# Optimization experiments

Measured on AMD Instinct MI355X. Metric: run time of the kernel, lower is better.

The kernel has to match this reference:

```python
import jax, jax.numpy as jnp
import numpy as np
from jax import lax

B, N, NPOINT = 16, 4096, 512
C_FEAT = 64
RADII = (0.2, 0.4)
NSAMPLES = (32, 64)
LAYER_DIMS = ([64, 64, 128], [64, 96, 128])  # hidden dims + feat_size per scale
C_IN = C_FEAT + 3  # use_xyz_feature=True prepends relative xyz
EPS = 1e-5


def setup_inputs() -> dict:
    key = jax.random.key(0)
    ks = jax.random.split(key, 32)
    inp = {
        "xyz": jax.random.uniform(ks[0], (B, N, 3), jnp.float32),
        "features": jax.random.normal(ks[1], (B, C_FEAT, N), jnp.float32),
    }
    ki = 2
    for s, dims in enumerate(LAYER_DIMS):
        full = [C_IN] + list(dims)
        for l in range(len(full) - 1):
            cin, cout = full[l], full[l + 1]
            inp["w_%d_%d" % (s, l)] = jax.random.normal(ks[ki], (cout, cin), jnp.float32) * np.float32(1.0 / np.sqrt(cin))
            inp["b_%d_%d" % (s, l)] = jnp.zeros((cout,), jnp.float32)
            inp["g_%d_%d" % (s, l)] = jnp.ones((cout,), jnp.float32)
            inp["beta_%d_%d" % (s, l)] = jnp.zeros((cout,), jnp.float32)
            ki += 1
    return inp


def _fps(xyz, npoint):
    # iterative farthest point sampling -> (B, npoint) int32 indices
    b, n, _ = xyz.shape
    init_idx = jnp.zeros((b,), jnp.int32)
    d0 = jnp.full((b, n), 1e10, xyz.dtype)

    def body(carry, _):
        dists, last = carry
        p = jnp.take_along_axis(xyz, last[:, None, None], axis=1)  # (B,1,3)
        dists = jnp.minimum(dists, jnp.sum((xyz - p) ** 2, -1))
        nxt = jnp.argmax(dists, -1).astype(jnp.int32)
        return (dists, nxt), nxt

    _, rest = lax.scan(body, (d0, init_idx), None, length=npoint - 1)
    return jnp.concatenate([init_idx[None, :], rest], 0).T


def _ball_query(xyz, new_xyz, radius, nsample):
    # first-nsample-in-order ball query, padded with first hit (CUDA ball_query semantics)
    n = xyz.shape[1]
    d2 = jnp.sum((new_xyz[:, :, None, :] - xyz[:, None, :, :]) ** 2, -1)  # (B,S,N)
    cand = jnp.where(d2 < radius * radius, jnp.arange(n, dtype=jnp.int32)[None, None, :], n)
    idx = jnp.sort(cand, axis=-1)[..., :nsample]
    first = idx[..., :1]
    idx = jnp.where(idx == n, first, idx)
    return jnp.minimum(idx, n - 1)


def _gather_pts(pts, idx):
    # pts (B,N,D), idx (B,...) -> (B,...,D)
    return jax.vmap(lambda p, i: p[i])(pts, idx)


def _scale(xyz, new_xyz, features, radius, nsample, params):
    idx = _ball_query(xyz, new_xyz, radius, nsample)  # (B,S,K)
    g_xyz = _gather_pts(xyz, idx) - new_xyz[:, :, None, :]  # (B,S,K,3) relative coords
    g_feat = jax.vmap(lambda f, i: f[:, i])(features, idx)  # (B,C,S,K)
    x = jnp.concatenate([g_xyz, jnp.transpose(g_feat, (0, 2, 3, 1))], -1)  # (B,S,K,3+C)
    nl = len(params)
    for li, (w, bb, gg, bt) in enumerate(params):
        # Conv1d(k=1) == per-point linear; BatchNorm1d train-mode stats over (batch*group, sample)
        x = jnp.einsum('bskc,oc->bsko', x, w) + bb
        mu = x.mean((0, 1, 2))
        var = x.var((0, 1, 2))
        x = (x - mu) * (gg / jnp.sqrt(var + EPS)) + bt
        if li < nl - 1:
            x = jax.nn.relu(x)
    # per-group max pool over samples -> (B,Cout,S)
    return jnp.transpose(x.max(2), (0, 2, 1))


def _forward(xyz, features, params_all):
    fps_idx = _fps(xyz, NPOINT)
    new_xyz = _gather_pts(xyz, fps_idx)  # (B,NPOINT,3)
    outs = [_scale(xyz, new_xyz, features, RADII[s], NSAMPLES[s], params_all[s]) for s in range(len(RADII))]
    return new_xyz, jnp.concatenate(outs, 1)  # (B,NPOINT,3), (B,256,NPOINT)


def reference(xyz, features,
              w_0_0, b_0_0, g_0_0, beta_0_0,
              w_0_1, b_0_1, g_0_1, beta_0_1,
              w_0_2, b_0_2, g_0_2, beta_0_2,
              w_1_0, b_1_0, g_1_0, beta_1_0,
              w_1_1, b_1_1, g_1_1, beta_1_1,
              w_1_2, b_1_2, g_1_2, beta_1_2):
    p0 = [(w_0_0, b_0_0, g_0_0, beta_0_0), (w_0_1, b_0_1, g_0_1, beta_0_1), (w_0_2, b_0_2, g_0_2, beta_0_2)]
    p1 = [(w_1_0, b_1_0, g_1_0, beta_1_0), (w_1_1, b_1_1, g_1_1, beta_1_1), (w_1_2, b_1_2, g_1_2, beta_1_2)]
    return _forward(xyz, features, [p0, p1])
```

## Files before the change

### kernel.cpp

```cpp
#include <hip/hip_runtime.h>

#define DEV __device__ __forceinline__

namespace {

typedef __attribute__((ext_vector_type(8))) short short8;
typedef __attribute__((ext_vector_type(4))) float f32x4;
typedef __attribute__((ext_vector_type(2))) float f32x2;

constexpr int B_ = 16, N_ = 4096, S_ = 512, CF_ = 64;
constexpr float EPS_ = 1e-5f;

constexpr int IDX0_OFF  = 0;
constexpr int IDX1_OFF  = 262144;
constexpr int STATS_OFF = IDX1_OFF + 524288;
constexpr int AC_OFF    = STATS_OFF + 49152;
constexpr int WP_OFF    = AC_OFF + 1536;
constexpr int MAXT_OFF  = WP_OFF + 21504;
constexpr int FEATT_OFF = MAXT_OFF + 1048576;
constexpr int Y0_OFF    = FEATT_OFF + 2097152;
constexpr int Y1_OFF    = Y0_OFF + 16777216;
constexpr size_t WS_NEED_FT   = (size_t)Y0_OFF * 4;
constexpr size_t WS_NEED_PIPE = (size_t)(Y1_OFF + 25165824) * 4;

constexpr int WP00 = 0,     WP01 = 6144,  WP02 = 10240;
constexpr int WP10 = 18432, WP11 = 24576, WP12 = 30720;

DEV int rfl(int x) { return __builtin_amdgcn_readfirstlane(x); }

DEV unsigned short f2bf(float x) {
  unsigned u = __float_as_uint(x);
  u += 0x7fff + ((u >> 16) & 1);
  return (unsigned short)(u >> 16);
}
DEV float bf2f(unsigned short u) { return __uint_as_float((unsigned)u << 16); }

DEV float dpp_max64(float v) {
  int m;
  m = __builtin_amdgcn_update_dpp(__float_as_int(v), __float_as_int(v), 0xB1, 0xf, 0xf, false);
  v = fmaxf(v, __int_as_float(m));
  m = __builtin_amdgcn_update_dpp(__float_as_int(v), __float_as_int(v), 0x4E, 0xf, 0xf, false);
  v = fmaxf(v, __int_as_float(m));
  m = __builtin_amdgcn_update_dpp(__float_as_int(v), __float_as_int(v), 0x141, 0xf, 0xf, false);
  v = fmaxf(v, __int_as_float(m));
  m = __builtin_amdgcn_update_dpp(__float_as_int(v), __float_as_int(v), 0x140, 0xf, 0xf, false);
  v = fmaxf(v, __int_as_float(m));
  m = __builtin_amdgcn_update_dpp(__float_as_int(v), __float_as_int(v), 0x142, 0xa, 0xf, false);
  v = fmaxf(v, __int_as_float(m));
  m = __builtin_amdgcn_update_dpp(__float_as_int(v), __float_as_int(v), 0x143, 0xc, 0xf, false);
  v = fmaxf(v, __int_as_float(m));
  return v;
}

__global__ __launch_bounds__(256) void fps_kernel(const float* __restrict__ xyz,
                                                  float* __restrict__ newxyz) {
  __shared__ float px[N_], py[N_], pz[N_];
  __shared__ unsigned long long swk[2][4];
  __shared__ int seq[S_];
  const int b = blockIdx.x, t = threadIdx.x;
  const int lane = t & 63, wv = t >> 6;
  const float* xb = xyz + (size_t)b * N_ * 3;
  for (int i = t; i < N_; i += 256) {
    px[i] = xb[i * 3 + 0];
    py[i] = xb[i * 3 + 1];
    pz[i] = xb[i * 3 + 2];
  }
  __syncthreads();
  f32x2 Xp[8], Yp[8], Zp[8], Dp[8];
#pragma unroll
  for (int jp = 0; jp < 8; ++jp) {
    Xp[jp] = *reinterpret_cast<const f32x2*>(&px[t * 16 + jp * 2]);
    Yp[jp] = *reinterpret_cast<const f32x2*>(&py[t * 16 + jp * 2]);
    Zp[jp] = *reinterpret_cast<const f32x2*>(&pz[t * 16 + jp * 2]);
    Dp[jp] = f32x2{1e10f, 1e10f};
  }
  float cx = px[0], cy = py[0], cz = pz[0];
  if (t == 0) seq[0] = 0;
  for (int it = 1; it < S_; ++it) {
    const int p = it & 1;
    f32x2 bvp = {-1.0f, -1.0f};
    {
#pragma clang fp contract(off)
      const f32x2 c2x = {cx, cx}, c2y = {cy, cy}, c2z = {cz, cz};
#pragma unroll
      for (int jp = 0; jp < 8; ++jp) {
        const f32x2 dx = Xp[jp] - c2x, dy = Yp[jp] - c2y, dz = Zp[jp] - c2z;
        const f32x2 d = (dx * dx + dy * dy) + dz * dz;
        Dp[jp] = __builtin_elementwise_min(Dp[jp], d);
        bvp = __builtin_elementwise_max(bvp, Dp[jp]);
      }
    }
    const float bv = fmaxf(bvp.x, bvp.y);
    int bj = 0;
#pragma unroll
    for (int j = 15; j >= 0; --j) {
      const float dj = Dp[j >> 1][j & 1];
      bj = (dj == bv) ? j : bj;
    }
    const int bi = t * 16 + bj;
    const float mxl = dpp_max64(bv);
    const float mx = __int_as_float(__builtin_amdgcn_readlane(__float_as_int(mxl), 63));
    const unsigned long long tie = __ballot(bv == mx);
    const int srcLane = (int)__builtin_ctzll(tie);
    const int wbi = __builtin_amdgcn_readlane(bi, srcLane);
    if (lane == 0)
      swk[p][wv] = ((unsigned long long)__float_as_uint(mx) << 32) | (unsigned)(~wbi);
    __syncthreads();
    const unsigned long long k0 = swk[p][0], k1 = swk[p][1];
    const unsigned long long k2 = swk[p][2], k3 = swk[p][3];
    const unsigned long long ka = k0 > k1 ? k0 : k1;
    const unsigned long long kb = k2 > k3 ? k2 : k3;
    const unsigned long long kw = ka > kb ? ka : kb;
    const int ri = (int)(~(unsigned)kw);
    cx = px[ri]; cy = py[ri]; cz = pz[ri];
    if (t == 0) seq[it] = ri;
  }
  __syncthreads();
  for (int i = t; i < S_; i += 256) {
    const int ri = seq[i];
    newxyz[(size_t)(b * S_ + i) * 3 + 0] = px[ri];
    newxyz[(size_t)(b * S_ + i) * 3 + 1] = py[ri];
    newxyz[(size_t)(b * S_ + i) * 3 + 2] = pz[ri];
  }
}

__global__ __launch_bounds__(256) void ballq_both(const float* __restrict__ xyz,
                                                  const float* __restrict__ newxyz,
                                                  int* __restrict__ idx0,
                                                  int* __restrict__ idx1) {
  __shared__ int sbuf[4][64];
  const int blk = blockIdx.x;
  const int scale = blk >> 11;
  const int cb = blk & 2047;
  const int NS = scale ? 64 : 32;
  const float r2 = scale ? 0.4f * 0.4f : 0.2f * 0.2f;
  int* __restrict__ idx = scale ? idx1 : idx0;
  const int wiv = threadIdx.x >> 6;
  const int lane = threadIdx.x & 63;
  const int cs = cb * 4 + wiv;
  const int b = cs >> 9;
  const float cx = newxyz[(size_t)cs * 3 + 0];
  const float cy = newxyz[(size_t)cs * 3 + 1];
  const float cz = newxyz[(size_t)cs * 3 + 2];
  const float* xb = xyz + (size_t)b * N_ * 3;
  int* my = sbuf[wiv];
  int cnt = 0;
  for (int base = 0; base < N_; base += 64) {
    if (cnt >= NS) break;
    const int i = base + lane;
    float d;
    {
#pragma clang fp contract(off)
      float dx = xb[i * 3 + 0] - cx, dy = xb[i * 3 + 1] - cy, dz = xb[i * 3 + 2] - cz;
      d = (dx * dx + dy * dy) + dz * dz;
    }
    const bool q = d < r2;
    const unsigned long long m = __ballot(q);
    if (q) {
      int pos = cnt + __popcll(m & ((1ull << lane) - 1ull));
      if (pos < NS) my[pos] = i;
    }
    cnt += __popcll(m);
  }
  __syncthreads();
  const int c = cnt < NS ? cnt : NS;
  const int first = my[0];
  for (int j = lane; j < NS; j += 64) idx[(size_t)cs * NS + j] = (j < c) ? my[j] : first;
}

__global__ __launch_bounds__(256) void prep_kernel(
    const float* __restrict__ feat, unsigned short* __restrict__ featT, int doFT,
    const float* __restrict__ w00, const float* __restrict__ w01, const float* __restrict__ w02,
    const float* __restrict__ w10, const float* __restrict__ w11, const float* __restrict__ w12,
    unsigned short* __restrict__ wp, float* __restrict__ stats) {
  const int blk = blockIdx.x, t = threadIdx.x;
  if (blk < 24) {
    for (int i = blk * 2048 + t; i < (blk + 1) * 2048; i += 256) stats[i] = 0.f;
  }
  {
    const int id = blk * 256 + t;
    const float* w = nullptr; int off = 0, KK = 0, CINW = 0, base = 0; bool perm = false;
    if (id < 768)       { w = w00; off = WP00; KK = 3; CINW = 67; perm = true;  base = 0; }
    else if (id < 1280) { w = w01; off = WP01; KK = 2; CINW = 64; perm = false; base = 768; }
    else if (id < 2304) { w = w02; off = WP02; KK = 2; CINW = 64; perm = false; base = 1280; }
    else if (id < 3072) { w = w10; off = WP10; KK = 3; CINW = 67; perm = true;  base = 2304; }
    else if (id < 3840) { w = w11; off = WP11; KK = 2; CINW = 64; perm = false; base = 3072; }
    else if (id < 5376) { w = w12; off = WP12; KK = 3; CINW = 96; perm = false; base = 3840; }
    if (w) {
      const int lid = id - base;
      const int lane = lid & 63, fr = lid >> 6;
      const int kk = fr % KK, nt = fr / KK;
      const int ccol = nt * 16 + (lane & 15);
      const int kbase = kk * 32 + (lane >> 4) * 8;
      unsigned short* dst = wp + off + (size_t)lid * 8;
#pragma unroll
      for (int j = 0; j < 8; ++j) {
        const int k = kbase + j;
        int cin;
        if (perm) cin = (k < 64) ? k + 3 : (k < 67 ? k - 64 : -1);
        else      cin = (k < CINW) ? k : -1;
        float f = (cin >= 0) ? w[ccol * CINW + cin] : 0.f;
        dst[j] = f2bf(f);
      }
    }
  }
  if (doFT) {
    __shared__ unsigned short tile[64][65];
    const int b = blk >> 6, nc = blk & 63;
    const int n0 = nc * 64;
    for (int i = t; i < 64 * 64; i += 256) {
      int c = i >> 6, n = i & 63;
      tile[c][n] = f2bf(feat[((size_t)b * CF_ + c) * N_ + n0 + n]);
    }
    __syncthreads();
    for (int i = t; i < 64 * 64; i += 256) {
      int n = i >> 6, c = i & 63;
      featT[((size_t)b * N_ + n0 + n) * 64 + c] = tile[c][n];
    }
  }
}

template <int DS>
DEV void flush_stats(const float* ssum, const float* ssq, int lane, int slot,
                     float* __restrict__ sg) {
  constexpr int NTS = DS / 16;
  float* dst = sg + (size_t)slot * 256;
#pragma unroll
  for (int nt = 0; nt < NTS; ++nt) {
    float s = ssum[nt], q = ssq[nt];
    s += __shfl_xor(s, 16); q += __shfl_xor(q, 16);
    s += __shfl_xor(s, 32); q += __shfl_xor(q, 32);
    if (lane < 16) {
      atomicAdd(&dst[nt * 16 + lane], s);
      atomicAdd(&dst[DS + nt * 16 + lane], q);
    }
  }
}

DEV void reduce_stats_block(const float* __restrict__ sg, float* sstats, int t) {
  float s = 0.f;
#pragma unroll
  for (int c = 0; c < 32; ++c) s += sg[c * 256 + t];
  sstats[t] = s;
  __syncthreads();
}

template <int K>
__global__ __launch_bounds__(256) void p1_kernel(
    const float* __restrict__ xyz, const unsigned short* __restrict__ featT,
    const float* __restrict__ newxyz, const int* __restrict__ idx,
    const unsigned short* __restrict__ wp0, const float* __restrict__ b0,
    unsigned short* __restrict__ y0, float* __restrict__ stats_out) {
  const int t = threadIdx.x, lane = t & 63;
  const int col = lane & 15, khi = lane >> 4;
  const int wid = rfl(t >> 6);
  constexpr int MT = (B_ * S_ * K) / 16;
  const int w0 = blockIdx.x * 4 + wid;
  short8 bfr[12];
#pragma unroll
  for (int i = 0; i < 12; ++i)
    bfr[i] = *reinterpret_cast<const short8*>(wp0 + ((size_t)i * 64 + lane) * 8);
  float bb[4];
#pragma unroll
  for (int nt = 0; nt < 4; ++nt) bb[nt] = b0[nt * 16 + col];
  float ssum[4] = {0.f, 0.f, 0.f, 0.f}, ssq[4] = {0.f, 0.f, 0.f, 0.f};
  for (int mt = w0; mt < MT; mt += 8192) {
    const int row = mt * 16 + col;
    const int cs = row / K;
    const int b = cs >> 9;
    const int pi = idx[row];
    const unsigned short* fr = featT + (((size_t)b * N_ + pi) << 6);
    const short8 a0 = *reinterpret_cast<const short8*>(fr + khi * 8);
    const short8 a1 = *reinterpret_cast<const short8*>(fr + 32 + khi * 8);
    short8 a2 = {0, 0, 0, 0, 0, 0, 0, 0};
    if (khi == 0) {
      const float* P = xyz + ((size_t)b * N_ + pi) * 3;
      const float* C = newxyz + (size_t)cs * 3;
      a2[0] = (short)f2bf(P[0] - C[0]);
      a2[1] = (short)f2bf(P[1] - C[1]);
      a2[2] = (short)f2bf(P[2] - C[2]);
    }
#pragma unroll
    for (int nt = 0; nt < 4; ++nt) {
      f32x4 a = {0.f, 0.f, 0.f, 0.f};
      a = __builtin_amdgcn_mfma_f32_16x16x32_bf16(a0, bfr[nt * 3 + 0], a, 0, 0, 0);
      a = __builtin_amdgcn_mfma_f32_16x16x32_bf16(a1, bfr[nt * 3 + 1], a, 0, 0, 0);
      a = __builtin_amdgcn_mfma_f32_16x16x32_bf16(a2, bfr[nt * 3 + 2], a, 0, 0, 0);
#pragma unroll
      for (int j = 0; j < 4; ++j) {
        const float y = a[j] + bb[nt];
        ssum[nt] += y; ssq[nt] += y * y;
        y0[(size_t)(mt * 16 + khi * 4 + j) * 64 + nt * 16 + col] = f2bf(y);
      }
    }
  }
  flush_stats<64>(ssum, ssq, lane, w0 & 31, stats_out);
}

template <int DIN, int DOUT>
__global__ __launch_bounds__(256) void p2_kernel(
    const unsigned short* __restrict__ yin, const unsigned short* __restrict__ wp,
    const float* __restrict__ bias, const float* __restrict__ gprev,
    const float* __restrict__ bprev, const float* __restrict__ stats_prev, float n,
    unsigned short* __restrict__ yout, float* __restrict__ stats_out, int MT) {
  constexpr int KK = DIN / 32, NT = DOUT / 16;
  __shared__ float sstats[256];
  const int t = threadIdx.x, lane = t & 63;
  const int col = lane & 15, khi = lane >> 4;
  const int wid = rfl(t >> 6);
  const int w0 = blockIdx.x * 4 + wid;
  reduce_stats_block(stats_prev, sstats, t);
  short8 bfr[NT * KK];
#pragma unroll
  for (int i = 0; i < NT * KK; ++i)
    bfr[i] = *reinterpret_cast<const short8*>(wp + ((size_t)i * 64 + lane) * 8);
  float bb[NT];
#pragma unroll
  for (int nt = 0; nt < NT; ++nt) bb[nt] = bias[nt * 16 + col];
  float ar[KK][8], cr[KK][8];
#pragma unroll
  for (int kk = 0; kk < KK; ++kk)
#pragma unroll
    for (int j = 0; j < 8; ++j) {
      const int ch = kk * 32 + khi * 8 + j;
      const float mu = sstats[ch] / n;
      const float var = sstats[DIN + ch] / n - mu * mu;
      const float a = gprev[ch] / sqrtf(var + EPS_);
      ar[kk][j] = a;
      cr[kk][j] = bprev[ch] - mu * a;
    }
  float ssum[NT], ssq[NT];
#pragma unroll
  for (int nt = 0; nt < NT; ++nt) { ssum[nt] = 0.f; ssq[nt] = 0.f; }
  for (int mt = w0; mt < MT; mt += 8192) {
    const size_t rb = (size_t)(mt * 16 + col) * DIN;
    short8 af[KK];
#pragma unroll
    for (int kk = 0; kk < KK; ++kk) {
      const short8 raw = *reinterpret_cast<const short8*>(yin + rb + kk * 32 + khi * 8);
#pragma unroll
      for (int j = 0; j < 8; ++j) {
        const float v = bf2f((unsigned short)raw[j]) * ar[kk][j] + cr[kk][j];
        af[kk][j] = (short)f2bf(fmaxf(v, 0.f));
      }
    }
#pragma unroll
    for (int nt = 0; nt < NT; ++nt) {
      f32x4 a = {0.f, 0.f, 0.f, 0.f};
#pragma unroll
      for (int kk = 0; kk < KK; ++kk)
        a = __builtin_amdgcn_mfma_f32_16x16x32_bf16(af[kk], bfr[nt * KK + kk], a, 0, 0, 0);
#pragma unroll
      for (int j = 0; j < 4; ++j) {
        const float y = a[j] + bb[nt];
        ssum[nt] += y; ssq[nt] += y * y;
        yout[(size_t)(mt * 16 + khi * 4 + j) * DOUT + nt * 16 + col] = f2bf(y);
      }
    }
  }
  flush_stats<DOUT>(ssum, ssq, lane, w0 & 31, stats_out);
}

template <int DIN, int K>
__global__ __launch_bounds__(256) void p3_kernel(
    const unsigned short* __restrict__ yin, const unsigned short* __restrict__ wp,
    const float* __restrict__ bias, const float* __restrict__ gprev,
    const float* __restrict__ bprev, const float* __restrict__ stats_prev, float n,
    float* __restrict__ maxtmp, float* __restrict__ stats_out) {
  constexpr int KK = DIN / 32, NT = 8;
  __shared__ float sstats[256];
  const int t = threadIdx.x, lane = t & 63;
  const int col = lane & 15, khi = lane >> 4;
  const int wid = rfl(t >> 6);
  const int c = blockIdx.x * 4 + wid;
  reduce_stats_block(stats_prev, sstats, t);
  short8 bfr[NT * KK];
#pragma unroll
  for (int i = 0; i < NT * KK; ++i)
    bfr[i] = *reinterpret_cast<const short8*>(wp + ((size_t)i * 64 + lane) * 8);
  float bb[NT];
#pragma unroll
  for (int nt = 0; nt < NT; ++nt) bb[nt] = bias[nt * 16 + col];
  float ar[KK][8], cr[KK][8];
#pragma unroll
  for (int kk = 0; kk < KK; ++kk)
#pragma unroll
    for (int j = 0; j < 8; ++j) {
      const int ch = kk * 32 + khi * 8 + j;
      const float mu = sstats[ch] / n;
      const float var = sstats[DIN + ch] / n - mu * mu;
      const float a = gprev[ch] / sqrtf(var + EPS_);
      ar[kk][j] = a;
      cr[kk][j] = bprev[ch] - mu * a;
    }
  float ssum[NT], ssq[NT], mx[NT];
#pragma unroll
  for (int nt = 0; nt < NT; ++nt) { ssum[nt] = 0.f; ssq[nt] = 0.f; mx[nt] = -3.4e38f; }
#pragma unroll
  for (int m = 0; m < K / 16; ++m) {
    const size_t rb = (size_t)(c * K + m * 16 + col) * DIN;
    short8 af[KK];
#pragma unroll
    for (int kk = 0; kk < KK; ++kk) {
      const short8 raw = *reinterpret_cast<const short8*>(yin + rb + kk * 32 + khi * 8);
#pragma unroll
      for (int j = 0; j < 8; ++j) {
        const float v = bf2f((unsigned short)raw[j]) * ar[kk][j] + cr[kk][j];
        af[kk][j] = (short)f2bf(fmaxf(v, 0.f));
      }
    }
#pragma unroll
    for (int nt = 0; nt < NT; ++nt) {
      f32x4 a = {0.f, 0.f, 0.f, 0.f};
#pragma unroll
      for (int kk = 0; kk < KK; ++kk)
        a = __builtin_amdgcn_mfma_f32_16x16x32_bf16(af[kk], bfr[nt * KK + kk], a, 0, 0, 0);
#pragma unroll
      for (int j = 0; j < 4; ++j) {
        const float y = a[j] + bb[nt];
        ssum[nt] += y; ssq[nt] += y * y;
        mx[nt] = fmaxf(mx[nt], y);
      }
    }
  }
#pragma unroll
  for (int nt = 0; nt < NT; ++nt) {
    mx[nt] = fmaxf(mx[nt], __shfl_xor(mx[nt], 16));
    mx[nt] = fmaxf(mx[nt], __shfl_xor(mx[nt], 32));
  }
  if (lane < 16) {
#pragma unroll
    for (int nt = 0; nt < NT; ++nt) maxtmp[(size_t)c * 128 + nt * 16 + lane] = mx[nt];
  }
  flush_stats<128>(ssum, ssq, lane, c & 31, stats_out);
}

__global__ __launch_bounds__(256) void out_kernel(const float* __restrict__ maxtmp,
                                                  const float* __restrict__ stats2,
                                                  const float* __restrict__ g2,
                                                  const float* __restrict__ be2, float n,
                                                  float* __restrict__ outf, int coff) {
  __shared__ float sstats[256];
  const int t = threadIdx.x;
  reduce_stats_block(stats2, sstats, t);
  const int i = blockIdx.x * 256 + t;
  if (i >= B_ * 128 * S_) return;
  const int s = i & 511;
  const int o = (i >> 9) & 127;
  const int b = i >> 16;
  const float mu = sstats[o] / n;
  const float var = sstats[128 + o] / n - mu * mu;
  const float a = g2[o] / sqrtf(var + EPS_);
  const float c = be2[o] - mu * a;
  const float v = maxtmp[((size_t)(b * S_ + s)) * 128 + o];
  outf[((size_t)b * 256 + coff + o) * S_ + s] = a * v + c;
}

template <int K, bool FT>
DEV void gather_tile(unsigned short* sX, const float* __restrict__ xyz,
                     const float* __restrict__ feat, const unsigned short* __restrict__ featT,
                     const float* __restrict__ newxyz, const int* __restrict__ idx, int tile) {
  const int t = threadIdx.x, r = t & 63, c4 = t >> 6;
  const int rep = r / K, k = r % K;
  const int cs = tile * (64 / K) + rep, b = cs >> 9;
  const int pi = idx[(size_t)cs * K + k];
  unsigned short* dst = sX + r * 104;
  if (FT) {
    const unsigned short* src = featT + (((size_t)b * N_ + pi) << 6) + c4 * 16;
    *reinterpret_cast<short8*>(dst + c4 * 16)     = *reinterpret_cast<const short8*>(src);
    *reinterpret_cast<short8*>(dst + c4 * 16 + 8) = *reinterpret_cast<const short8*>(src + 8);
  } else {
#pragma unroll
    for (int j = 0; j < 16; ++j) {
      const int ch = c4 * 16 + j;
      dst[ch] = f2bf(feat[((size_t)b * CF_ + ch) * N_ + pi]);
    }
  }
  if (c4 == 0) {
    const float* P = xyz + ((size_t)b * N_ + pi) * 3;
    const float* C = newxyz + (size_t)cs * 3;
    dst[64] = f2bf(P[0] - C[0]);
    dst[65] = f2bf(P[1] - C[1]);
    dst[66] = f2bf(P[2] - C[2]);
  }
}

template <int NTILES, int KK>
DEV void layer_mfma(const unsigned short* sIn, int stride, const unsigned short* __restrict__ wp,
                    int lane, int wid, f32x4* acc) {
  short8 af[KK];
  const int arow = wid * 16 + (lane & 15);
  const int kof = (lane >> 4) * 8;
#pragma unroll
  for (int kk = 0; kk < KK; ++kk)
    af[kk] = *reinterpret_cast<const short8*>(sIn + arow * stride + kk * 32 + kof);
#pragma unroll
  for (int nt = 0; nt < NTILES; ++nt) {
    f32x4 a = {0.f, 0.f, 0.f, 0.f};
#pragma unroll
    for (int kk = 0; kk < KK; ++kk) {
      short8 bf = *reinterpret_cast<const short8*>(wp + ((size_t)(nt * KK + kk) * 64 + lane) * 8);
      a = __builtin_amdgcn_mfma_f32_16x16x32_bf16(af[kk], bf, a, 0, 0, 0);
    }
    acc[nt] = a;
  }
}

template <int K, int D0, int D1, int D2, int STAGE, bool FT>
__global__ __launch_bounds__(256) void stage_mfma(
    const float* __restrict__ xyz, const float* __restrict__ feat,
    const unsigned short* __restrict__ featT, const float* __restrict__ newxyz,
    const int* __restrict__ idx,
    const unsigned short* __restrict__ wp0, const unsigned short* __restrict__ wp1,
    const unsigned short* __restrict__ wp2,
    const float* __restrict__ b0, const float* __restrict__ b1, const float* __restrict__ b2,
    const float* __restrict__ ac0, const float* __restrict__ ac1,
    float* __restrict__ stats_out, float* __restrict__ maxtmp) {
  constexpr int CPB = 64 / K, NT = (B_ * S_) / CPB;
  constexpr int ST0 = 104, ST1 = 72, ST2 = (D1 == 96) ? 104 : 72;
  constexpr int KK0 = 3, KK1 = D0 / 32, KK2 = D1 / 32;
  constexpr int NT0 = D0 / 16, NT1 = D1 / 16, NT2 = D2 / 16;
  constexpr int DS = (STAGE == 1) ? D0 : (STAGE == 2) ? D1 : D2;
  constexpr int NTS = DS / 16;

  __shared__ unsigned short sX[64 * ST0];
  __shared__ unsigned short sY0[(STAGE >= 2) ? 64 * ST1 : 8];
  __shared__ unsigned short sY1[(STAGE == 3) ? 64 * ST2 : 8];
  __shared__ float smax[(STAGE == 3) ? 512 : 4];

  const int t = threadIdx.x, lane = t & 63;
  const int wid = rfl(t >> 6);
  const int col = lane & 15, khi = lane >> 4;

  for (int i = t; i < 64 * 37; i += 256) sX[(i / 37) * ST0 + 67 + (i % 37)] = 0;

  float b0r[NT0], a0r[NT0], c0r[NT0];
  float b1r[NT1], a1r[NT1], c1r[NT1];
  float b2r[NT2];
#pragma unroll
  for (int nt = 0; nt < NT0; ++nt) {
    b0r[nt] = b0[nt * 16 + col];
    if constexpr (STAGE >= 2) {
      a0r[nt] = ac0[nt * 16 + col];
      c0r[nt] = ac0[D0 + nt * 16 + col];
    }
  }
  if constexpr (STAGE >= 2) {
#pragma unroll
    for (int nt = 0; nt < NT1; ++nt) {
      b1r[nt] = b1[nt * 16 + col];
      if constexpr (STAGE == 3) {
        a1r[nt] = ac1[nt * 16 + col];
        c1r[nt] = ac1[D1 + nt * 16 + col];
      }
    }
  }
  if constexpr (STAGE == 3) {
#pragma unroll
    for (int nt = 0; nt < NT2; ++nt) b2r[nt] = b2[nt * 16 + col];
  }

  float ssum[NTS], ssq[NTS];
#pragma unroll
  for (int nt = 0; nt < NTS; ++nt) { ssum[nt] = 0.f; ssq[nt] = 0.f; }

  for (int tile = blockIdx.x; tile < NT; tile += gridDim.x) {
    __syncthreads();
    gather_tile<K, FT>(sX, xyz, feat, featT, newxyz, idx, tile);
    __syncthreads();

    f32x4 acc0[NT0];
    layer_mfma<NT0, KK0>(sX, ST0, wp0, lane, wid, acc0);
    if constexpr (STAGE == 1) {
#pragma unroll
      for (int nt = 0; nt < NT0; ++nt) {
        const float bb = b0r[nt];
#pragma unroll
        for (int j = 0; j < 4; ++j) {
          const float y = acc0[nt][j] + bb;
          ssum[nt] += y; ssq[nt] += y * y;
        }
      }
    } else {
#pragma unroll
      for (int nt = 0; nt < NT0; ++nt) {
#pragma unroll
        for (int j = 0; j < 4; ++j) {
          float y = (acc0[nt][j] + b0r[nt]) * a0r[nt] + c0r[nt];
          y = fmaxf(y, 0.f);
          sY0[(wid * 16 + khi * 4 + j) * ST1 + nt * 16 + col] = f2bf(y);
        }
      }
      __syncthreads();
      f32x4 acc1[NT1];
      layer_mfma<NT1, KK1>(sY0, ST1, wp1, lane, wid, acc1);
      if constexpr (STAGE == 2) {
#pragma unroll
        for (int nt = 0; nt < NT1; ++nt) {
          const float bb = b1r[nt];
#pragma unroll
          for (int j = 0; j < 4; ++j) {
            const float y = acc1[nt][j] + bb;
            ssum[nt] += y; ssq[nt] += y * y;
          }
        }
      } else {
#pragma unroll
        for (int nt = 0; nt < NT1; ++nt) {
#pragma unroll
          for (int j = 0; j < 4; ++j) {
            float y = (acc1[nt][j] + b1r[nt]) * a1r[nt] + c1r[nt];
            y = fmaxf(y, 0.f);
            sY1[(wid * 16 + khi * 4 + j) * ST2 + nt * 16 + col] = f2bf(y);
          }
        }
        __syncthreads();
        f32x4 acc2[NT2];
        layer_mfma<NT2, KK2>(sY1, ST2, wp2, lane, wid, acc2);
#pragma unroll
        for (int nt = 0; nt < NT2; ++nt) {
          const float bb = b2r[nt];
          const float y0 = acc2[nt][0] + bb, y1 = acc2[nt][1] + bb;
          const float y2 = acc2[nt][2] + bb, y3 = acc2[nt][3] + bb;
          ssum[nt] += (y0 + y1) + (y2 + y3);
          ssq[nt] += (y0 * y0 + y1 * y1) + (y2 * y2 + y3 * y3);
          float m = fmaxf(fmaxf(y0, y1), fmaxf(y2, y3));
          m = fmaxf(m, __shfl_xor(m, 16));
          m = fmaxf(m, __shfl_xor(m, 32));
          if (lane < 16) smax[wid * 128 + nt * 16 + lane] = m;
        }
        __syncthreads();
        if constexpr (K == 64) {
          if (t < 128) {
            const float m = fmaxf(fmaxf(smax[t], smax[128 + t]), fmaxf(smax[256 + t], smax[384 + t]));
            maxtmp[(size_t)tile * 128 + t] = m;
          }
        } else {
          const int ce = t >> 7, ch = t & 127;
          const float m = fmaxf(smax[ce * 256 + ch], smax[ce * 256 + 128 + ch]);
          maxtmp[((size_t)(tile * 2 + ce)) * 128 + ch] = m;
        }
      }
    }
  }
  flush_stats<DS>(ssum, ssq, lane, (int)(blockIdx.x * 4 + wid) & 31, stats_out);
}

__global__ void finalize_kernel(const float* __restrict__ stats, const float* __restrict__ g,
                                const float* __restrict__ beta, float* __restrict__ ac,
                                float n, int cout) {
  const int t = threadIdx.x;
  if (t < cout) {
    float s = 0.f, q = 0.f;
#pragma unroll
    for (int c = 0; c < 32; ++c) {
      s += stats[c * 256 + t];
      q += stats[c * 256 + cout + t];
    }
    const float mu = s / n;
    const float var = q / n - mu * mu;
    const float a = g[t] / sqrtf(var + EPS_);
    ac[t] = a;
    ac[cout + t] = beta[t] - mu * a;
  }
}

}

extern "C" void kernel_launch(void* const* d_in, const int* in_sizes, int n_in,
                              void* d_out, int out_size, void* d_ws, size_t ws_size,
                              hipStream_t stream) {
  const float* xyz  = (const float*)d_in[0];
  const float* feat = (const float*)d_in[1];
  const float* w00 = (const float*)d_in[2];  const float* b00 = (const float*)d_in[3];
  const float* g00 = (const float*)d_in[4];  const float* be00 = (const float*)d_in[5];
  const float* w01 = (const float*)d_in[6];  const float* b01 = (const float*)d_in[7];
  const float* g01 = (const float*)d_in[8];  const float* be01 = (const float*)d_in[9];
  const float* w02 = (const float*)d_in[10]; const float* b02 = (const float*)d_in[11];
  const float* g02 = (const float*)d_in[12]; const float* be02 = (const float*)d_in[13];
  const float* w10 = (const float*)d_in[14]; const float* b10 = (const float*)d_in[15];
  const float* g10 = (const float*)d_in[16]; const float* be10 = (const float*)d_in[17];
  const float* w11 = (const float*)d_in[18]; const float* b11 = (const float*)d_in[19];
  const float* g11 = (const float*)d_in[20]; const float* be11 = (const float*)d_in[21];
  const float* w12 = (const float*)d_in[22]; const float* b12 = (const float*)d_in[23];
  const float* g12 = (const float*)d_in[24]; const float* be12 = (const float*)d_in[25];

  float* ws = (float*)d_ws;
  int* idx0 = (int*)(ws + IDX0_OFF);
  int* idx1 = (int*)(ws + IDX1_OFF);
  float* stats = ws + STATS_OFF;
  float* ac = ws + AC_OFF;
  unsigned short* wp = (unsigned short*)(ws + WP_OFF);
  float* maxtmp = ws + MAXT_OFF;
  unsigned short* featT = (unsigned short*)(ws + FEATT_OFF);
  unsigned short* y0us = (unsigned short*)(ws + Y0_OFF);
  unsigned short* y1us = (unsigned short*)(ws + Y1_OFF);

  const bool usePipe = ws_size >= WS_NEED_PIPE;
  const bool useFT   = ws_size >= WS_NEED_FT;

  float* outF = (float*)d_out;
  float* outFeat = outF + B_ * S_ * 3;

  prep_kernel<<<1024, 256, 0, stream>>>(feat, featT, useFT ? 1 : 0,
                                        w00, w01, w02, w10, w11, w12, wp, stats);
  fps_kernel<<<16, 256, 0, stream>>>(xyz, outF);
  ballq_both<<<4096, 256, 0, stream>>>(xyz, outF, idx0, idx1);

  const float n0 = (float)(B_ * S_ * 32);
  const float n1 = (float)(B_ * S_ * 64);
  float* st0 = stats + 0 * 8192;
  float* st1 = stats + 1 * 8192;
  float* st2 = stats + 2 * 8192;
  float* st3 = stats + 3 * 8192;
  float* st4 = stats + 4 * 8192;
  float* st5 = stats + 5 * 8192;

  if (usePipe) {
    p1_kernel<32><<<2048, 256, 0, stream>>>(xyz, featT, outF, idx0, wp + WP00, b00,
                                            y0us, st0);
    p2_kernel<64, 64><<<2048, 256, 0, stream>>>(y0us, wp + WP01, b01, g00, be00,
                                                st0, n0, y1us, st1, 16384);
    p3_kernel<64, 32><<<2048, 256, 0, stream>>>(y1us, wp + WP02, b02, g01, be01,
                                                st1, n0, maxtmp, st2);
    out_kernel<<<4096, 256, 0, stream>>>(maxtmp, st2, g02, be02, n0, outFeat, 0);

    p1_kernel<64><<<2048, 256, 0, stream>>>(xyz, featT, outF, idx1, wp + WP10, b10,
                                            y0us, st3);
    p2_kernel<64, 96><<<2048, 256, 0, stream>>>(y0us, wp + WP11, b11, g10, be10,
                                                st3, n1, y1us, st4, 32768);
    p3_kernel<96, 64><<<2048, 256, 0, stream>>>(y1us, wp + WP12, b12, g11, be11,
                                                st4, n1, maxtmp, st5);
    out_kernel<<<4096, 256, 0, stream>>>(maxtmp, st5, g12, be12, n1, outFeat, 128);
    return;
  }

#define LAUNCH_SCALE0(STG, ST)                                                          \
  do {                                                                                  \
    if (useFT)                                                                          \
      stage_mfma<32, 64, 64, 128, STG, true><<<2048, 256, 0, stream>>>(                 \
          xyz, feat, featT, outF, idx0, wp + WP00, wp + WP01, wp + WP02, b00, b01, b02, \
          ac + 0 * 256, ac + 1 * 256, ST, maxtmp);                                      \
    else                                                                                \
      stage_mfma<32, 64, 64, 128, STG, false><<<2048, 256, 0, stream>>>(                \
          xyz, feat, featT, outF, idx0, wp + WP00, wp + WP01, wp + WP02, b00, b01, b02, \
          ac + 0 * 256, ac + 1 * 256, ST, maxtmp);                                      \
  } while (0)
#define LAUNCH_SCALE1(STG, ST)                                                          \
  do {                                                                                  \
    if (useFT)                                                                          \
      stage_mfma<64, 64, 96, 128, STG, true><<<2048, 256, 0, stream>>>(                 \
          xyz, feat, featT, outF, idx1, wp + WP10, wp + WP11, wp + WP12, b10, b11, b12, \
          ac + 3 * 256, ac + 4 * 256, ST, maxtmp);                                      \
    else                                                                                \
      stage_mfma<64, 64, 96, 128, STG, false><<<2048, 256, 0, stream>>>(                \
          xyz, feat, featT, outF, idx1, wp + WP10, wp + WP11, wp + WP12, b10, b11, b12, \
          ac + 3 * 256, ac + 4 * 256, ST, maxtmp);                                      \
  } while (0)

  LAUNCH_SCALE0(1, st0);
  finalize_kernel<<<1, 128, 0, stream>>>(st0, g00, be00, ac + 0 * 256, n0, 64);
  LAUNCH_SCALE0(2, st1);
  finalize_kernel<<<1, 128, 0, stream>>>(st1, g01, be01, ac + 1 * 256, n0, 64);
  LAUNCH_SCALE0(3, st2);
  out_kernel<<<4096, 256, 0, stream>>>(maxtmp, st2, g02, be02, n0, outFeat, 0);

  LAUNCH_SCALE1(1, st3);
  finalize_kernel<<<1, 128, 0, stream>>>(st3, g10, be10, ac + 3 * 256, n1, 64);
  LAUNCH_SCALE1(2, st4);
  finalize_kernel<<<1, 128, 0, stream>>>(st4, g11, be11, ac + 4 * 256, n1, 96);
  LAUNCH_SCALE1(3, st5);
  out_kernel<<<4096, 256, 0, stream>>>(maxtmp, st5, g12, be12, n1, outFeat, 128);

#undef LAUNCH_SCALE0
#undef LAUNCH_SCALE1
}
```

Baseline: 547.0 us.

## Fuse ball query and MLP stages into one cooperative persistent kernel

```diff
diff --git a/kernel.cpp b/kernel.cpp
--- a/kernel.cpp
+++ b/kernel.cpp
@@ -1,6 +1,9 @@
 #include <hip/hip_runtime.h>
+#include <hip/hip_cooperative_groups.h>
 
 #define DEV __device__ __forceinline__
+
+namespace cg = cooperative_groups;
 
 namespace {
 
@@ -20,11 +23,13 @@
 constexpr int FEATT_OFF = MAXT_OFF + 1048576;
 constexpr int Y0_OFF    = FEATT_OFF + 2097152;
 constexpr int Y1_OFF    = Y0_OFF + 16777216;
-constexpr size_t WS_NEED_FT   = (size_t)Y0_OFF * 4;
 constexpr size_t WS_NEED_PIPE = (size_t)(Y1_OFF + 25165824) * 4;
 
 constexpr int WP00 = 0,     WP01 = 6144,  WP02 = 10240;
 constexpr int WP10 = 18432, WP11 = 24576, WP12 = 30720;
+
+constexpr float N0F = (float)(B_ * S_ * 32);
+constexpr float N1F = (float)(B_ * S_ * 64);
 
 DEV int rfl(int x) { return __builtin_amdgcn_readfirstlane(x); }
 
@@ -124,52 +129,8 @@
   }
 }
 
-__global__ __launch_bounds__(256) void ballq_both(const float* __restrict__ xyz,
-                                                  const float* __restrict__ newxyz,
-                                                  int* __restrict__ idx0,
-                                                  int* __restrict__ idx1) {
-  __shared__ int sbuf[4][64];
-  const int blk = blockIdx.x;
-  const int scale = blk >> 11;
-  const int cb = blk & 2047;
-  const int NS = scale ? 64 : 32;
-  const float r2 = scale ? 0.4f * 0.4f : 0.2f * 0.2f;
-  int* __restrict__ idx = scale ? idx1 : idx0;
-  const int wiv = threadIdx.x >> 6;
-  const int lane = threadIdx.x & 63;
-  const int cs = cb * 4 + wiv;
-  const int b = cs >> 9;
-  const float cx = newxyz[(size_t)cs * 3 + 0];
-  const float cy = newxyz[(size_t)cs * 3 + 1];
-  const float cz = newxyz[(size_t)cs * 3 + 2];
-  const float* xb = xyz + (size_t)b * N_ * 3;
-  int* my = sbuf[wiv];
-  int cnt = 0;
-  for (int base = 0; base < N_; base += 64) {
-    if (cnt >= NS) break;
-    const int i = base + lane;
-    float d;
-    {
-#pragma clang fp contract(off)
-      float dx = xb[i * 3 + 0] - cx, dy = xb[i * 3 + 1] - cy, dz = xb[i * 3 + 2] - cz;
-      d = (dx * dx + dy * dy) + dz * dz;
-    }
-    const bool q = d < r2;
-    const unsigned long long m = __ballot(q);
-    if (q) {
-      int pos = cnt + __popcll(m & ((1ull << lane) - 1ull));
-      if (pos < NS) my[pos] = i;
-    }
-    cnt += __popcll(m);
-  }
-  __syncthreads();
-  const int c = cnt < NS ? cnt : NS;
-  const int first = my[0];
-  for (int j = lane; j < NS; j += 64) idx[(size_t)cs * NS + j] = (j < c) ? my[j] : first;
-}
-
 __global__ __launch_bounds__(256) void prep_kernel(
-    const float* __restrict__ feat, unsigned short* __restrict__ featT, int doFT,
+    const float* __restrict__ feat, unsigned short* __restrict__ featT,
     const float* __restrict__ w00, const float* __restrict__ w01, const float* __restrict__ w02,
     const float* __restrict__ w10, const float* __restrict__ w11, const float* __restrict__ w12,
     unsigned short* __restrict__ wp, float* __restrict__ stats) {
@@ -204,7 +165,7 @@
       }
     }
   }
-  if (doFT) {
+  {
     __shared__ unsigned short tile[64][65];
     const int b = blk >> 6, nc = blk & 63;
     const int n0 = nc * 64;
@@ -245,17 +206,56 @@
   __syncthreads();
 }
 
+DEV void ballq_dev(const float* __restrict__ xyz, const float* __restrict__ newxyz,
+                   int* __restrict__ idx0, int* __restrict__ idx1,
+                   int (*sbuf)[64], int gw, int NW) {
+  const int lane = threadIdx.x & 63;
+  const int wiv = threadIdx.x >> 6;
+  int* my = sbuf[wiv];
+  for (int csp = gw; csp < 16384; csp += NW) {
+    const int scale = csp >> 13;
+    const int cs = csp & 8191;
+    const int NS = scale ? 64 : 32;
+    const float r2 = scale ? 0.4f * 0.4f : 0.2f * 0.2f;
+    int* __restrict__ idx = scale ? idx1 : idx0;
+    const int b = cs >> 9;
+    const float cx = newxyz[(size_t)cs * 3 + 0];
+    const float cy = newxyz[(size_t)cs * 3 + 1];
+    const float cz = newxyz[(size_t)cs * 3 + 2];
+    const float* xb = xyz + (size_t)b * N_ * 3;
+    int cnt = 0;
+    for (int base = 0; base < N_; base += 64) {
+      if (cnt >= NS) break;
+      const int i = base + lane;
+      float d;
+      {
+#pragma clang fp contract(off)
+        float dx = xb[i * 3 + 0] - cx, dy = xb[i * 3 + 1] - cy, dz = xb[i * 3 + 2] - cz;
+        d = (dx * dx + dy * dy) + dz * dz;
+      }
+      const bool q = d < r2;
+      const unsigned long long m = __ballot(q);
+      if (q) {
+        int pos = cnt + __popcll(m & ((1ull << lane) - 1ull));
+        if (pos < NS) my[pos] = i;
+      }
+      cnt += __popcll(m);
+    }
+    const int c = cnt < NS ? cnt : NS;
+    const int first = my[0];
+    for (int j = lane; j < NS; j += 64) idx[(size_t)cs * NS + j] = (j < c) ? my[j] : first;
+  }
+}
+
 template <int K>
-__global__ __launch_bounds__(256) void p1_kernel(
-    const float* __restrict__ xyz, const unsigned short* __restrict__ featT,
-    const float* __restrict__ newxyz, const int* __restrict__ idx,
-    const unsigned short* __restrict__ wp0, const float* __restrict__ b0,
-    unsigned short* __restrict__ y0, float* __restrict__ stats_out) {
-  const int t = threadIdx.x, lane = t & 63;
+DEV void p1_dev(const float* __restrict__ xyz, const unsigned short* __restrict__ featT,
+                const float* __restrict__ newxyz, const int* __restrict__ idx,
+                const unsigned short* __restrict__ wp0, const float* __restrict__ b0,
+                unsigned short* __restrict__ y0, float* __restrict__ stats_out,
+                int gw, int NW) {
+  const int lane = threadIdx.x & 63;
   const int col = lane & 15, khi = lane >> 4;
-  const int wid = rfl(t >> 6);
   constexpr int MT = (B_ * S_ * K) / 16;
-  const int w0 = blockIdx.x * 4 + wid;
   short8 bfr[12];
 #pragma unroll
   for (int i = 0; i < 12; ++i)
@@ -264,7 +264,7 @@
 #pragma unroll
   for (int nt = 0; nt < 4; ++nt) bb[nt] = b0[nt * 16 + col];
   float ssum[4] = {0.f, 0.f, 0.f, 0.f}, ssq[4] = {0.f, 0.f, 0.f, 0.f};
-  for (int mt = w0; mt < MT; mt += 8192) {
+  for (int mt = gw; mt < MT; mt += NW) {
     const int row = mt * 16 + col;
     const int cs = row / K;
     const int b = cs >> 9;
@@ -294,21 +294,18 @@
       }
     }
   }
-  flush_stats<64>(ssum, ssq, lane, w0 & 31, stats_out);
+  flush_stats<64>(ssum, ssq, lane, gw & 31, stats_out);
 }
 
 template <int DIN, int DOUT>
-__global__ __launch_bounds__(256) void p2_kernel(
-    const unsigned short* __restrict__ yin, const unsigned short* __restrict__ wp,
-    const float* __restrict__ bias, const float* __restrict__ gprev,
-    const float* __restrict__ bprev, const float* __restrict__ stats_prev, float n,
-    unsigned short* __restrict__ yout, float* __restrict__ stats_out, int MT) {
+DEV void p2_dev(const unsigned short* __restrict__ yin, const unsigned short* __restrict__ wp,
+                const float* __restrict__ bias, const float* __restrict__ gprev,
+                const float* __restrict__ bprev, const float* __restrict__ stats_prev, float n,
+                unsigned short* __restrict__ yout, float* __restrict__ stats_out, int MT,
+                float* sstats, int gw, int NW) {
   constexpr int KK = DIN / 32, NT = DOUT / 16;
-  __shared__ float sstats[256];
   const int t = threadIdx.x, lane = t & 63;
   const int col = lane & 15, khi = lane >> 4;
-  const int wid = rfl(t >> 6);
-  const int w0 = blockIdx.x * 4 + wid;
   reduce_stats_block(stats_prev, sstats, t);
   short8 bfr[NT * KK];
 #pragma unroll
@@ -332,7 +329,7 @@
   float ssum[NT], ssq[NT];
 #pragma unroll
   for (int nt = 0; nt < NT; ++nt) { ssum[nt] = 0.f; ssq[nt] = 0.f; }
-  for (int mt = w0; mt < MT; mt += 8192) {
+  for (int mt = gw; mt < MT; mt += NW) {
     const size_t rb = (size_t)(mt * 16 + col) * DIN;
     short8 af[KK];
 #pragma unroll
@@ -358,26 +355,19 @@
       }
     }
   }
-  flush_stats<DOUT>(ssum, ssq, lane, w0 & 31, stats_out);
+  flush_stats<DOUT>(ssum, ssq, lane, gw & 31, stats_out);
 }
 
 template <int DIN, int K>
-__global__ __launch_bounds__(256) void p3_kernel(
-    const unsigned short* __restrict__ yin, const unsigned short* __restrict__ wp,
-    const float* __restrict__ bias, const float* __restrict__ gprev,
-    const float* __restrict__ bprev, const float* __restrict__ stats_prev, float n,
-    float* __restrict__ maxtmp, float* __restrict__ stats_out) {
+DEV void p3_dev(const unsigned short* __restrict__ yin, const unsigned short* __restrict__ wp,
+                const float* __restrict__ bias, const float* __restrict__ gprev,
+                const float* __restrict__ bprev, const float* __restrict__ stats_prev, float n,
+                float* __restrict__ maxtmp, float* __restrict__ stats_out,
+                float* sstats, int gw, int NW) {
   constexpr int KK = DIN / 32, NT = 8;
-  __shared__ float sstats[256];
   const int t = threadIdx.x, lane = t & 63;
   const int col = lane & 15, khi = lane >> 4;
-  const int wid = rfl(t >> 6);
-  const int c = blockIdx.x * 4 + wid;
   reduce_stats_block(stats_prev, sstats, t);
-  short8 bfr[NT * KK];
-#pragma unroll
-  for (int i = 0; i < NT * KK; ++i)
-    bfr[i] = *reinterpret_cast<const short8*>(wp + ((size_t)i * 64 + lane) * 8);
   float bb[NT];
 #pragma unroll
   for (int nt = 0; nt < NT; ++nt) bb[nt] = bias[nt * 16 + col];
@@ -393,46 +383,158 @@
       ar[kk][j] = a;
       cr[kk][j] = bprev[ch] - mu * a;
     }
-  float ssum[NT], ssq[NT], mx[NT];
-#pragma unroll
-  for (int nt = 0; nt < NT; ++nt) { ssum[nt] = 0.f; ssq[nt] = 0.f; mx[nt] = -3.4e38f; }
-#pragma unroll
-  for (int m = 0; m < K / 16; ++m) {
-    const size_t rb = (size_t)(c * K + m * 16 + col) * DIN;
-    short8 af[KK];
-#pragma unroll
-    for (int kk = 0; kk < KK; ++kk) {
-      const short8 raw = *reinterpret_cast<const short8*>(yin + rb + kk * 32 + khi * 8);
-#pragma unroll
-      for (int j = 0; j < 8; ++j) {
-        const float v = bf2f((unsigned short)raw[j]) * ar[kk][j] + cr[kk][j];
-        af[kk][j] = (short)f2bf(fmaxf(v, 0.f));
+  float ssum[NT], ssq[NT];
+#pragma unroll
+  for (int nt = 0; nt < NT; ++nt) { ssum[nt] = 0.f; ssq[nt] = 0.f; }
+  for (int c = gw; c < B_ * S_; c += NW) {
+    float mx[NT];
+#pragma unroll
+    for (int nt = 0; nt < NT; ++nt) mx[nt] = -3.4e38f;
+#pragma unroll
+    for (int m = 0; m < K / 16; ++m) {
+      const size_t rb = (size_t)(c * K + m * 16 + col) * DIN;
+      short8 af[KK];
+#pragma unroll
+      for (int kk = 0; kk < KK; ++kk) {
+        const short8 raw = *reinterpret_cast<const short8*>(yin + rb + kk * 32 + khi * 8);
+#pragma unroll
+        for (int j = 0; j < 8; ++j) {
+          const float v = bf2f((unsigned short)raw[j]) * ar[kk][j] + cr[kk][j];
+          af[kk][j] = (short)f2bf(fmaxf(v, 0.f));
+        }
+      }
+#pragma unroll
+      for (int nt = 0; nt < NT; ++nt) {
+        f32x4 a = {0.f, 0.f, 0.f, 0.f};
+#pragma unroll
+        for (int kk = 0; kk < KK; ++kk) {
+          const short8 bf =
+              *reinterpret_cast<const short8*>(wp + ((size_t)(nt * KK + kk) * 64 + lane) * 8);
+          a = __builtin_amdgcn_mfma_f32_16x16x32_bf16(af[kk], bf, a, 0, 0, 0);
+        }
+#pragma unroll
+        for (int j = 0; j < 4; ++j) {
+          const float y = a[j] + bb[nt];
+          ssum[nt] += y; ssq[nt] += y * y;
+          mx[nt] = fmaxf(mx[nt], y);
+        }
       }
     }
 #pragma unroll
     for (int nt = 0; nt < NT; ++nt) {
-      f32x4 a = {0.f, 0.f, 0.f, 0.f};
-#pragma unroll
-      for (int kk = 0; kk < KK; ++kk)
-        a = __builtin_amdgcn_mfma_f32_16x16x32_bf16(af[kk], bfr[nt * KK + kk], a, 0, 0, 0);
-#pragma unroll
-      for (int j = 0; j < 4; ++j) {
-        const float y = a[j] + bb[nt];
-        ssum[nt] += y; ssq[nt] += y * y;
-        mx[nt] = fmaxf(mx[nt], y);
-      }
-    }
-  }
-#pragma unroll
-  for (int nt = 0; nt < NT; ++nt) {
-    mx[nt] = fmaxf(mx[nt], __shfl_xor(mx[nt], 16));
-    mx[nt] = fmaxf(mx[nt], __shfl_xor(mx[nt], 32));
-  }
-  if (lane < 16) {
-#pragma unroll
-    for (int nt = 0; nt < NT; ++nt) maxtmp[(size_t)c * 128 + nt * 16 + lane] = mx[nt];
-  }
-  flush_stats<128>(ssum, ssq, lane, c & 31, stats_out);
+      mx[nt] = fmaxf(mx[nt], __shfl_xor(mx[nt], 16));
+      mx[nt] = fmaxf(mx[nt], __shfl_xor(mx[nt], 32));
+    }
+    if (lane < 16) {
+#pragma unroll
+      for (int nt = 0; nt < NT; ++nt) maxtmp[(size_t)c * 128 + nt * 16 + lane] = mx[nt];
+    }
+  }
+  flush_stats<128>(ssum, ssq, lane, gw & 31, stats_out);
+}
+
+DEV void out_dev(const float* __restrict__ maxtmp, const float* __restrict__ stats2,
+                 const float* __restrict__ g2, const float* __restrict__ be2, float n,
+                 float* __restrict__ outf, int coff, float* sstats) {
+  const int t = threadIdx.x;
+  reduce_stats_block(stats2, sstats, t);
+  const int stride = gridDim.x * 256;
+  for (int i = blockIdx.x * 256 + t; i < B_ * 128 * S_; i += stride) {
+    const int s = i & 511;
+    const int o = (i >> 9) & 127;
+    const int b = i >> 16;
+    const float mu = sstats[o] / n;
+    const float var = sstats[128 + o] / n - mu * mu;
+    const float a = g2[o] / sqrtf(var + EPS_);
+    const float c = be2[o] - mu * a;
+    const float v = maxtmp[((size_t)(b * S_ + s)) * 128 + o];
+    outf[((size_t)b * 256 + coff + o) * S_ + s] = a * v + c;
+  }
+  __syncthreads();
+}
+
+__global__ __launch_bounds__(256, 4) void mega_kernel(
+    const float* __restrict__ xyz, const unsigned short* __restrict__ featT,
+    const float* __restrict__ newxyz, int* __restrict__ idx0, int* __restrict__ idx1,
+    const unsigned short* __restrict__ wp,
+    const float* __restrict__ b00, const float* __restrict__ g00, const float* __restrict__ be00,
+    const float* __restrict__ b01, const float* __restrict__ g01, const float* __restrict__ be01,
+    const float* __restrict__ b02, const float* __restrict__ g02, const float* __restrict__ be02,
+    const float* __restrict__ b10, const float* __restrict__ g10, const float* __restrict__ be10,
+    const float* __restrict__ b11, const float* __restrict__ g11, const float* __restrict__ be11,
+    const float* __restrict__ b12, const float* __restrict__ g12, const float* __restrict__ be12,
+    unsigned short* __restrict__ y0, unsigned short* __restrict__ y1,
+    float* __restrict__ maxtmp, float* __restrict__ stats, float* __restrict__ outFeat) {
+  cg::grid_group grid = cg::this_grid();
+  __shared__ float sstats[256];
+  __shared__ int sbuf[4][64];
+  const int t = threadIdx.x;
+  const int wid = rfl(t >> 6);
+  const int gw = blockIdx.x * 4 + wid;
+  const int NW = gridDim.x * 4;
+
+  ballq_dev(xyz, newxyz, idx0, idx1, sbuf, gw, NW);
+  grid.sync();
+  p1_dev<32>(xyz, featT, newxyz, idx0, wp + WP00, b00, y0, stats + 0 * 8192, gw, NW);
+  grid.sync();
+  p2_dev<64, 64>(y0, wp + WP01, b01, g00, be00, stats + 0 * 8192, N0F, y1, stats + 1 * 8192,
+                 16384, sstats, gw, NW);
+  grid.sync();
+  p3_dev<64, 32>(y1, wp + WP02, b02, g01, be01, stats + 1 * 8192, N0F, maxtmp,
+                 stats + 2 * 8192, sstats, gw, NW);
+  grid.sync();
+  out_dev(maxtmp, stats + 2 * 8192, g02, be02, N0F, outFeat, 0, sstats);
+  p1_dev<64>(xyz, featT, newxyz, idx1, wp + WP10, b10, y0, stats + 3 * 8192, gw, NW);
+  grid.sync();
+  p2_dev<64, 96>(y0, wp + WP11, b11, g10, be10, stats + 3 * 8192, N1F, y1, stats + 4 * 8192,
+                 32768, sstats, gw, NW);
+  grid.sync();
+  p3_dev<96, 64>(y1, wp + WP12, b12, g11, be11, stats + 4 * 8192, N1F, maxtmp,
+                 stats + 5 * 8192, sstats, gw, NW);
+  grid.sync();
+  out_dev(maxtmp, stats + 5 * 8192, g12, be12, N1F, outFeat, 128, sstats);
+}
+
+__global__ __launch_bounds__(256) void ballq_both(const float* __restrict__ xyz,
+                                                  const float* __restrict__ newxyz,
+                                                  int* __restrict__ idx0,
+                                                  int* __restrict__ idx1) {
+  __shared__ int sbuf[4][64];
+  const int gw = blockIdx.x * 4 + rfl(threadIdx.x >> 6);
+  ballq_dev(xyz, newxyz, idx0, idx1, sbuf, gw, 16384);
+}
+
+template <int K>
+__global__ __launch_bounds__(256) void p1_kernel(
+    const float* __restrict__ xyz, const unsigned short* __restrict__ featT,
+    const float* __restrict__ newxyz, const int* __restrict__ idx,
+    const unsigned short* __restrict__ wp0, const float* __restrict__ b0,
+    unsigned short* __restrict__ y0, float* __restrict__ stats_out) {
+  const int gw = blockIdx.x * 4 + rfl(threadIdx.x >> 6);
+  p1_dev<K>(xyz, featT, newxyz, idx, wp0, b0, y0, stats_out, gw, 8192);
+}
+
+template <int DIN, int DOUT>
+__global__ __launch_bounds__(256) void p2_kernel(
+    const unsigned short* __restrict__ yin, const unsigned short* __restrict__ wp,
+    const float* __restrict__ bias, const float* __restrict__ gprev,
+    const float* __restrict__ bprev, const float* __restrict__ stats_prev, float n,
+    unsigned short* __restrict__ yout, float* __restrict__ stats_out, int MT) {
+  __shared__ float sstats[256];
+  const int gw = blockIdx.x * 4 + rfl(threadIdx.x >> 6);
+  p2_dev<DIN, DOUT>(yin, wp, bias, gprev, bprev, stats_prev, n, yout, stats_out, MT, sstats,
+                    gw, 8192);
+}
+
+template <int DIN, int K>
+__global__ __launch_bounds__(256) void p3_kernel(
+    const unsigned short* __restrict__ yin, const unsigned short* __restrict__ wp,
+    const float* __restrict__ bias, const float* __restrict__ gprev,
+    const float* __restrict__ bprev, const float* __restrict__ stats_prev, float n,
+    float* __restrict__ maxtmp, float* __restrict__ stats_out) {
+  __shared__ float sstats[256];
+  const int gw = blockIdx.x * 4 + rfl(threadIdx.x >> 6);
+  p3_dev<DIN, K>(yin, wp, bias, gprev, bprev, stats_prev, n, maxtmp, stats_out, sstats, gw, 8192);
 }
 
 __global__ __launch_bounds__(256) void out_kernel(const float* __restrict__ maxtmp,
@@ -441,228 +543,7 @@
                                                   const float* __restrict__ be2, float n,
                                                   float* __restrict__ outf, int coff) {
   __shared__ float sstats[256];
-  const int t = threadIdx.x;
-  reduce_stats_block(stats2, sstats, t);
-  const int i = blockIdx.x * 256 + t;
-  if (i >= B_ * 128 * S_) return;
-  const int s = i & 511;
-  const int o = (i >> 9) & 127;
-  const int b = i >> 16;
-  const float mu = sstats[o] / n;
-  const float var = sstats[128 + o] / n - mu * mu;
-  const float a = g2[o] / sqrtf(var + EPS_);
-  const float c = be2[o] - mu * a;
-  const float v = maxtmp[((size_t)(b * S_ + s)) * 128 + o];
-  outf[((size_t)b * 256 + coff + o) * S_ + s] = a * v + c;
-}
-
-template <int K, bool FT>
-DEV void gather_tile(unsigned short* sX, const float* __restrict__ xyz,
-                     const float* __restrict__ feat, const unsigned short* __restrict__ featT,
-                     const float* __restrict__ newxyz, const int* __restrict__ idx, int tile) {
-  const int t = threadIdx.x, r = t & 63, c4 = t >> 6;
-  const int rep = r / K, k = r % K;
-  const int cs = tile * (64 / K) + rep, b = cs >> 9;
-  const int pi = idx[(size_t)cs * K + k];
-  unsigned short* dst = sX + r * 104;
-  if (FT) {
-    const unsigned short* src = featT + (((size_t)b * N_ + pi) << 6) + c4 * 16;
-    *reinterpret_cast<short8*>(dst + c4 * 16)     = *reinterpret_cast<const short8*>(src);
-    *reinterpret_cast<short8*>(dst + c4 * 16 + 8) = *reinterpret_cast<const short8*>(src + 8);
-  } else {
-#pragma unroll
-    for (int j = 0; j < 16; ++j) {
-      const int ch = c4 * 16 + j;
-      dst[ch] = f2bf(feat[((size_t)b * CF_ + ch) * N_ + pi]);
-    }
-  }
-  if (c4 == 0) {
-    const float* P = xyz + ((size_t)b * N_ + pi) * 3;
-    const float* C = newxyz + (size_t)cs * 3;
-    dst[64] = f2bf(P[0] - C[0]);
-    dst[65] = f2bf(P[1] - C[1]);
-    dst[66] = f2bf(P[2] - C[2]);
-  }
-}
-
-template <int NTILES, int KK>
-DEV void layer_mfma(const unsigned short* sIn, int stride, const unsigned short* __restrict__ wp,
-                    int lane, int wid, f32x4* acc) {
-  short8 af[KK];
-  const int arow = wid * 16 + (lane & 15);
-  const int kof = (lane >> 4) * 8;
-#pragma unroll
-  for (int kk = 0; kk < KK; ++kk)
-    af[kk] = *reinterpret_cast<const short8*>(sIn + arow * stride + kk * 32 + kof);
-#pragma unroll
-  for (int nt = 0; nt < NTILES; ++nt) {
-    f32x4 a = {0.f, 0.f, 0.f, 0.f};
-#pragma unroll
-    for (int kk = 0; kk < KK; ++kk) {
-      short8 bf = *reinterpret_cast<const short8*>(wp + ((size_t)(nt * KK + kk) * 64 + lane) * 8);
-      a = __builtin_amdgcn_mfma_f32_16x16x32_bf16(af[kk], bf, a, 0, 0, 0);
-    }
-    acc[nt] = a;
-  }
-}
-
-template <int K, int D0, int D1, int D2, int STAGE, bool FT>
-__global__ __launch_bounds__(256) void stage_mfma(
-    const float* __restrict__ xyz, const float* __restrict__ feat,
-    const unsigned short* __restrict__ featT, const float* __restrict__ newxyz,
-    const int* __restrict__ idx,
-    const unsigned short* __restrict__ wp0, const unsigned short* __restrict__ wp1,
-    const unsigned short* __restrict__ wp2,
-    const float* __restrict__ b0, const float* __restrict__ b1, const float* __restrict__ b2,
-    const float* __restrict__ ac0, const float* __restrict__ ac1,
-    float* __restrict__ stats_out, float* __restrict__ maxtmp) {
-  constexpr int CPB = 64 / K, NT = (B_ * S_) / CPB;
-  constexpr int ST0 = 104, ST1 = 72, ST2 = (D1 == 96) ? 104 : 72;
-  constexpr int KK0 = 3, KK1 = D0 / 32, KK2 = D1 / 32;
-  constexpr int NT0 = D0 / 16, NT1 = D1 / 16, NT2 = D2 / 16;
-  constexpr int DS = (STAGE == 1) ? D0 : (STAGE == 2) ? D1 : D2;
-  constexpr int NTS = DS / 16;
-
-  __shared__ unsigned short sX[64 * ST0];
-  __shared__ unsigned short sY0[(STAGE >= 2) ? 64 * ST1 : 8];
-  __shared__ unsigned short sY1[(STAGE == 3) ? 64 * ST2 : 8];
-  __shared__ float smax[(STAGE == 3) ? 512 : 4];
-
-  const int t = threadIdx.x, lane = t & 63;
-  const int wid = rfl(t >> 6);
-  const int col = lane & 15, khi = lane >> 4;
-
-  for (int i = t; i < 64 * 37; i += 256) sX[(i / 37) * ST0 + 67 + (i % 37)] = 0;
-
-  float b0r[NT0], a0r[NT0], c0r[NT0];
-  float b1r[NT1], a1r[NT1], c1r[NT1];
-  float b2r[NT2];
-#pragma unroll
-  for (int nt = 0; nt < NT0; ++nt) {
-    b0r[nt] = b0[nt * 16 + col];
-    if constexpr (STAGE >= 2) {
-      a0r[nt] = ac0[nt * 16 + col];
-      c0r[nt] = ac0[D0 + nt * 16 + col];
-    }
-  }
-  if constexpr (STAGE >= 2) {
-#pragma unroll
-    for (int nt = 0; nt < NT1; ++nt) {
-      b1r[nt] = b1[nt * 16 + col];
-      if constexpr (STAGE == 3) {
-        a1r[nt] = ac1[nt * 16 + col];
-        c1r[nt] = ac1[D1 + nt * 16 + col];
-      }
-    }
-  }
-  if constexpr (STAGE == 3) {
-#pragma unroll
-    for (int nt = 0; nt < NT2; ++nt) b2r[nt] = b2[nt * 16 + col];
-  }
-
-  float ssum[NTS], ssq[NTS];
-#pragma unroll
-  for (int nt = 0; nt < NTS; ++nt) { ssum[nt] = 0.f; ssq[nt] = 0.f; }
-
-  for (int tile = blockIdx.x; tile < NT; tile += gridDim.x) {
-    __syncthreads();
-    gather_tile<K, FT>(sX, xyz, feat, featT, newxyz, idx, tile);
-    __syncthreads();
-
-    f32x4 acc0[NT0];
-    layer_mfma<NT0, KK0>(sX, ST0, wp0, lane, wid, acc0);
-    if constexpr (STAGE == 1) {
-#pragma unroll
-      for (int nt = 0; nt < NT0; ++nt) {
-        const float bb = b0r[nt];
-#pragma unroll
-        for (int j = 0; j < 4; ++j) {
-          const float y = acc0[nt][j] + bb;
-          ssum[nt] += y; ssq[nt] += y * y;
-        }
-      }
-    } else {
-#pragma unroll
-      for (int nt = 0; nt < NT0; ++nt) {
-#pragma unroll
-        for (int j = 0; j < 4; ++j) {
-          float y = (acc0[nt][j] + b0r[nt]) * a0r[nt] + c0r[nt];
-          y = fmaxf(y, 0.f);
-          sY0[(wid * 16 + khi * 4 + j) * ST1 + nt * 16 + col] = f2bf(y);
-        }
-      }
-      __syncthreads();
-      f32x4 acc1[NT1];
-      layer_mfma<NT1, KK1>(sY0, ST1, wp1, lane, wid, acc1);
-      if constexpr (STAGE == 2) {
-#pragma unroll
-        for (int nt = 0; nt < NT1; ++nt) {
-          const float bb = b1r[nt];
-#pragma unroll
-          for (int j = 0; j < 4; ++j) {
-            const float y = acc1[nt][j] + bb;
-            ssum[nt] += y; ssq[nt] += y * y;
-          }
-        }
-      } else {
-#pragma unroll
-        for (int nt = 0; nt < NT1; ++nt) {
-#pragma unroll
-          for (int j = 0; j < 4; ++j) {
-            float y = (acc1[nt][j] + b1r[nt]) * a1r[nt] + c1r[nt];
-            y = fmaxf(y, 0.f);
-            sY1[(wid * 16 + khi * 4 + j) * ST2 + nt * 16 + col] = f2bf(y);
-          }
-        }
-        __syncthreads();
-        f32x4 acc2[NT2];
-        layer_mfma<NT2, KK2>(sY1, ST2, wp2, lane, wid, acc2);
-#pragma unroll
-        for (int nt = 0; nt < NT2; ++nt) {
-          const float bb = b2r[nt];
-          const float y0 = acc2[nt][0] + bb, y1 = acc2[nt][1] + bb;
-          const float y2 = acc2[nt][2] + bb, y3 = acc2[nt][3] + bb;
-          ssum[nt] += (y0 + y1) + (y2 + y3);
-          ssq[nt] += (y0 * y0 + y1 * y1) + (y2 * y2 + y3 * y3);
-          float m = fmaxf(fmaxf(y0, y1), fmaxf(y2, y3));
-          m = fmaxf(m, __shfl_xor(m, 16));
-          m = fmaxf(m, __shfl_xor(m, 32));
-          if (lane < 16) smax[wid * 128 + nt * 16 + lane] = m;
-        }
-        __syncthreads();
-        if constexpr (K == 64) {
-          if (t < 128) {
-            const float m = fmaxf(fmaxf(smax[t], smax[128 + t]), fmaxf(smax[256 + t], smax[384 + t]));
-            maxtmp[(size_t)tile * 128 + t] = m;
-          }
-        } else {
-          const int ce = t >> 7, ch = t & 127;
-          const float m = fmaxf(smax[ce * 256 + ch], smax[ce * 256 + 128 + ch]);
-          maxtmp[((size_t)(tile * 2 + ce)) * 128 + ch] = m;
-        }
-      }
-    }
-  }
-  flush_stats<DS>(ssum, ssq, lane, (int)(blockIdx.x * 4 + wid) & 31, stats_out);
-}
-
-__global__ void finalize_kernel(const float* __restrict__ stats, const float* __restrict__ g,
-                                const float* __restrict__ beta, float* __restrict__ ac,
-                                float n, int cout) {
-  const int t = threadIdx.x;
-  if (t < cout) {
-    float s = 0.f, q = 0.f;
-#pragma unroll
-    for (int c = 0; c < 32; ++c) {
-      s += stats[c * 256 + t];
-      q += stats[c * 256 + cout + t];
-    }
-    const float mu = s / n;
-    const float var = q / n - mu * mu;
-    const float a = g[t] / sqrtf(var + EPS_);
-    ac[t] = a;
-    ac[cout + t] = beta[t] - mu * a;
-  }
+  out_dev(maxtmp, stats2, g2, be2, n, outf, coff, sstats);
 }
 
 }
@@ -689,89 +570,52 @@
   int* idx0 = (int*)(ws + IDX0_OFF);
   int* idx1 = (int*)(ws + IDX1_OFF);
   float* stats = ws + STATS_OFF;
-  float* ac = ws + AC_OFF;
   unsigned short* wp = (unsigned short*)(ws + WP_OFF);
   float* maxtmp = ws + MAXT_OFF;
   unsigned short* featT = (unsigned short*)(ws + FEATT_OFF);
   unsigned short* y0us = (unsigned short*)(ws + Y0_OFF);
   unsigned short* y1us = (unsigned short*)(ws + Y1_OFF);
 
-  const bool usePipe = ws_size >= WS_NEED_PIPE;
-  const bool useFT   = ws_size >= WS_NEED_FT;
-
   float* outF = (float*)d_out;
   float* outFeat = outF + B_ * S_ * 3;
 
-  prep_kernel<<<1024, 256, 0, stream>>>(feat, featT, useFT ? 1 : 0,
-                                        w00, w01, w02, w10, w11, w12, wp, stats);
+  (void)ws_size;
+  prep_kernel<<<1024, 256, 0, stream>>>(feat, featT, w00, w01, w02, w10, w11, w12, wp, stats);
   fps_kernel<<<16, 256, 0, stream>>>(xyz, outF);
+
+  const float* newxyz_c = outF;
+  const unsigned short* featT_c = featT;
+  const unsigned short* wp_c = wp;
+  void* args[] = {
+      (void*)&xyz, (void*)&featT_c, (void*)&newxyz_c, (void*)&idx0, (void*)&idx1, (void*)&wp_c,
+      (void*)&b00, (void*)&g00, (void*)&be00,
+      (void*)&b01, (void*)&g01, (void*)&be01,
+      (void*)&b02, (void*)&g02, (void*)&be02,
+      (void*)&b10, (void*)&g10, (void*)&be10,
+      (void*)&b11, (void*)&g11, (void*)&be11,
+      (void*)&b12, (void*)&g12, (void*)&be12,
+      (void*)&y0us, (void*)&y1us, (void*)&maxtmp, (void*)&stats, (void*)&outFeat};
+  hipError_t err = hipLaunchCooperativeKernel((const void*)mega_kernel, dim3(1024), dim3(256),
+                                              args, 0, stream);
+  if (err == hipSuccess) return;
+
   ballq_both<<<4096, 256, 0, stream>>>(xyz, outF, idx0, idx1);
-
-  const float n0 = (float)(B_ * S_ * 32);
-  const float n1 = (float)(B_ * S_ * 64);
   float* st0 = stats + 0 * 8192;
   float* st1 = stats + 1 * 8192;
   float* st2 = stats + 2 * 8192;
   float* st3 = stats + 3 * 8192;
   float* st4 = stats + 4 * 8192;
   float* st5 = stats + 5 * 8192;
-
-  if (usePipe) {
-    p1_kernel<32><<<2048, 256, 0, stream>>>(xyz, featT, outF, idx0, wp + WP00, b00,
-                                            y0us, st0);
-    p2_kernel<64, 64><<<2048, 256, 0, stream>>>(y0us, wp + WP01, b01, g00, be00,
-                                                st0, n0, y1us, st1, 16384);
-    p3_kernel<64, 32><<<2048, 256, 0, stream>>>(y1us, wp + WP02, b02, g01, be01,
-                                                st1, n0, maxtmp, st2);
-    out_kernel<<<4096, 256, 0, stream>>>(maxtmp, st2, g02, be02, n0, outFeat, 0);
-
-    p1_kernel<64><<<2048, 256, 0, stream>>>(xyz, featT, outF, idx1, wp + WP10, b10,
-                                            y0us, st3);
-    p2_kernel<64, 96><<<2048, 256, 0, stream>>>(y0us, wp + WP11, b11, g10, be10,
-                                                st3, n1, y1us, st4, 32768);
-    p3_kernel<96, 64><<<2048, 256, 0, stream>>>(y1us, wp + WP12, b12, g11, be11,
-                                                st4, n1, maxtmp, st5);
-    out_kernel<<<4096, 256, 0, stream>>>(maxtmp, st5, g12, be12, n1, outFeat, 128);
-    return;
-  }
-
-#define LAUNCH_SCALE0(STG, ST)                                                          \
-  do {                                                                                  \
-    if (useFT)                                                                          \
-      stage_mfma<32, 64, 64, 128, STG, true><<<2048, 256, 0, stream>>>(                 \
-          xyz, feat, featT, outF, idx0, wp + WP00, wp + WP01, wp + WP02, b00, b01, b02, \
-          ac + 0 * 256, ac + 1 * 256, ST, maxtmp);                                      \
-    else                                                                                \
-      stage_mfma<32, 64, 64, 128, STG, false><<<2048, 256, 0, stream>>>(                \
-          xyz, feat, featT, outF, idx0, wp + WP00, wp + WP01, wp + WP02, b00, b01, b02, \
-          ac + 0 * 256, ac + 1 * 256, ST, maxtmp);                                      \
-  } while (0)
-#define LAUNCH_SCALE1(STG, ST)                                                          \
-  do {                                                                                  \
-    if (useFT)                                                                          \
-      stage_mfma<64, 64, 96, 128, STG, true><<<2048, 256, 0, stream>>>(                 \
-          xyz, feat, featT, outF, idx1, wp + WP10, wp + WP11, wp + WP12, b10, b11, b12, \
-          ac + 3 * 256, ac + 4 * 256, ST, maxtmp);                                      \
-    else                                                                                \
-      stage_mfma<64, 64, 96, 128, STG, false><<<2048, 256, 0, stream>>>(                \
-          xyz, feat, featT, outF, idx1, wp + WP10, wp + WP11, wp + WP12, b10, b11, b12, \
-          ac + 3 * 256, ac + 4 * 256, ST, maxtmp);                                      \
-  } while (0)
-
-  LAUNCH_SCALE0(1, st0);
-  finalize_kernel<<<1, 128, 0, stream>>>(st0, g00, be00, ac + 0 * 256, n0, 64);
-  LAUNCH_SCALE0(2, st1);
-  finalize_kernel<<<1, 128, 0, stream>>>(st1, g01, be01, ac + 1 * 256, n0, 64);
-  LAUNCH_SCALE0(3, st2);
-  out_kernel<<<4096, 256, 0, stream>>>(maxtmp, st2, g02, be02, n0, outFeat, 0);
-
-  LAUNCH_SCALE1(1, st3);
-  finalize_kernel<<<1, 128, 0, stream>>>(st3, g10, be10, ac + 3 * 256, n1, 64);
-  LAUNCH_SCALE1(2, st4);
-  finalize_kernel<<<1, 128, 0, stream>>>(st4, g11, be11, ac + 4 * 256, n1, 96);
-  LAUNCH_SCALE1(3, st5);
-  out_kernel<<<4096, 256, 0, stream>>>(maxtmp, st5, g12, be12, n1, outFeat, 128);
-
-#undef LAUNCH_SCALE0
-#undef LAUNCH_SCALE1
-}
+  p1_kernel<32><<<2048, 256, 0, stream>>>(xyz, featT, outF, idx0, wp + WP00, b00, y0us, st0);
+  p2_kernel<64, 64><<<2048, 256, 0, stream>>>(y0us, wp + WP01, b01, g00, be00, st0, N0F, y1us,
+                                              st1, 16384);
+  p3_kernel<64, 32><<<2048, 256, 0, stream>>>(y1us, wp + WP02, b02, g01, be01, st1, N0F, maxtmp,
+                                              st2);
+  out_kernel<<<4096, 256, 0, stream>>>(maxtmp, st2, g02, be02, N0F, outFeat, 0);
+  p1_kernel<64><<<2048, 256, 0, stream>>>(xyz, featT, outF, idx1, wp + WP10, b10, y0us, st3);
+  p2_kernel<64, 96><<<2048, 256, 0, stream>>>(y0us, wp + WP11, b11, g10, be10, st3, N1F, y1us,
+                                              st4, 32768);
+  p3_kernel<96, 64><<<2048, 256, 0, stream>>>(y1us, wp + WP12, b12, g11, be11, st4, N1F, maxtmp,
+                                              st5);
+  out_kernel<<<4096, 256, 0, stream>>>(maxtmp, st5, g12, be12, N1F, outFeat, 128);
+}
```

Result: slower. 1.844 ms (+237.1%).
